# Kernel optimization log

Hardware: AMD Instinct MI355X
Metric: run time of the kernel (lower is better)

The kernel has to match this reference:

```python
import jax, jax.numpy as jnp
import numpy as np

STATE_DIM = 64   # state_dim (N), N/2 complex modes
KLEN = 128       # L, learned impulse-response length
CH = 1           # channel_dim
BATCH = 32
T = 1048576      # sequence length (T > L -> FFT branch)
DT_MIN, DT_MAX = 0.001, 0.1


def setup_inputs() -> dict:
    key = jax.random.key(0)
    ks = jax.random.split(key, 7)
    N2 = STATE_DIM // 2
    x = jax.random.normal(ks[0], (BATCH, CH, T), dtype=jnp.float32)
    # HiPPO initialization: w = -0.5 + i * (1/pi) * N * (N/(1+2k) - 1)
    k = np.arange(N2)
    w_real = np.broadcast_to(np.float32(-0.5), (CH, N2)).copy()
    w_imag = np.broadcast_to(
        ((1.0 / np.pi) * STATE_DIM * (STATE_DIM / (1.0 + 2.0 * k) - 1.0)).astype(np.float32),
        (CH, N2)).copy()
    log_dt = (jax.random.uniform(ks[1], (CH, 1), dtype=jnp.float32)
              * (np.log(DT_MAX) - np.log(DT_MIN)) + np.log(DT_MIN))
    C_real = jax.random.normal(ks[2], (CH, 1, N2), dtype=jnp.float32) * 0.1
    C_imag = jax.random.normal(ks[3], (CH, 1, N2), dtype=jnp.float32) * 0.1
    B_real = jax.random.normal(ks[4], (CH, N2), dtype=jnp.float32)
    B_imag = jax.random.normal(ks[5], (CH, N2), dtype=jnp.float32)
    nrm = jnp.sqrt(jnp.sum(B_real ** 2 + B_imag ** 2, axis=-1, keepdims=True))
    B_real, B_imag = B_real / nrm, B_imag / nrm
    D = jax.random.normal(ks[6], (CH,), dtype=jnp.float32) * 0.1
    return {"azimuth_data": x,
            "w_real": jnp.asarray(w_real), "w_imag": jnp.asarray(w_imag),
            "log_dt": log_dt,
            "C_real": C_real, "C_imag": C_imag,
            "B_real": B_real, "B_imag": B_imag,
            "D": D}


def _ssm_kernel(w_real, w_imag, log_dt, C_real, C_imag, B_real, B_imag, D, L):
    """Vectorized equivalent of the per-step power recurrence: h_k = Re(sum_n C_n B_n A_n^k)."""
    w = w_real + 1j * w_imag                      # (CH, N2) complex eigenvalues
    dt = jnp.exp(log_dt)                          # (CH, 1)
    Cc = C_real + 1j * C_imag                     # (CH, 1, N2)
    Bc = B_real + 1j * B_imag                     # (CH, N2)
    dtA = dt[..., None] * w                       # (CH,1,1)*(CH,N2) -> (CH,1,N2)
    # coefficients C.squeeze(1) * B, with the same broadcast as torch: (CH,N2)*(CH,1,N2)->(CH,1,N2)
    coef = jnp.squeeze(Cc, axis=1) * (jnp.ones_like(dtA) * Bc)   # (CH,1,N2)
    ks = jnp.arange(L, dtype=dtA.real.dtype)                      # (L,)
    Ak = jnp.exp(dtA[..., None] * ks)                             # (CH,1,N2,L) = A_discrete**k
    h = jnp.real(jnp.sum(coef[..., None] * Ak, axis=-2))          # (CH,1,L)
    h = h.at[..., 0].add(D)                                       # hk[0] += D (broadcast (CH,1)+(CH,))
    return h[:, None]                                             # unsqueeze(1) -> (CH,1,1,L)


def reference(azimuth_data, w_real, w_imag, log_dt, C_real, C_imag, B_real, B_imag, D):
    Bsz, Cn, Tn = azimuth_data.shape
    kernel = _ssm_kernel(w_real, w_imag, log_dt, C_real, C_imag, B_real, B_imag, D, KLEN)
    pad = KLEN - 1
    x_padded = jnp.pad(azimuth_data, ((0, 0), (0, 0), (pad, 0)))   # causal left-pad
    L_conv = x_padded.shape[-1]
    x_f = jnp.fft.rfft(x_padded, n=L_conv)                         # (B, CH, F)
    k_f = jnp.fft.rfft(kernel, n=L_conv)                           # (CH, 1, 1, F)
    y_f = x_f * k_f                                                # broadcast -> (CH, B, 1, F)
    focused = jnp.fft.irfft(y_f, n=L_conv)[..., :Tn]               # (CH, B, 1, T) — matches torch broadcast
    return focused
```

## Files before the change

kernel.cpp:

```cpp
#include <hip/hip_runtime.h>

#define T_LEN  1048576
#define NROWS  32
#define NTAPS  128
#define N2     32
#define BLOCK  256
#define SEG    4096
#define SEGS_PER_ROW 256
#define HALO   256
#define NCH    11
#define STG_CH 1088

typedef __attribute__((ext_vector_type(8)))  _Float16 half8;
typedef __attribute__((ext_vector_type(2)))  __fp16   fp16x2;
typedef __attribute__((ext_vector_type(16))) float    f32x16;

__device__ __forceinline__ int swz(int q) { return q ^ ((q >> 3) & 7); }

__device__ __forceinline__ void gload_lds16(const float* g, float* l) {
  __builtin_amdgcn_global_load_lds(
      (const __attribute__((address_space(1))) void*)g,
      (__attribute__((address_space(3))) void*)l, 16, 0, 0);
}

__global__ __launch_bounds__(NTAPS) void ssm_taps(
    const float* __restrict__ w_real, const float* __restrict__ w_imag,
    const float* __restrict__ log_dt,
    const float* __restrict__ C_real, const float* __restrict__ C_imag,
    const float* __restrict__ B_real, const float* __restrict__ B_imag,
    const float* __restrict__ Dp, float* __restrict__ ws) {
  __shared__ float hsh[NTAPS];
  const int k = threadIdx.x;
  const float dt = expf(log_dt[0]);
  const float kf = (float)k;
  float acc = 0.f;
  for (int n = 0; n < N2; ++n) {
    const float a  = dt * w_real[n];
    const float b  = dt * w_imag[n];
    const float cr = C_real[n], ci = C_imag[n];
    const float br = B_real[n], bi = B_imag[n];
    const float coef_r = cr * br - ci * bi;
    const float coef_i = cr * bi + ci * br;
    const float e = expf(a * kf);
    float s, c;
    sincosf(b * kf, &s, &c);
    acc += e * (coef_r * c - coef_i * s);
  }
  if (k == 0) acc += Dp[0];
  ws[k]  = acc;
  hsh[k] = acc;
  __syncthreads();
  if (k < 64) {
    _Float16* AH = (_Float16*)(ws + NTAPS);
    const int m = k & 31, g = k >> 5;
    for (int c = 0; c < NCH; ++c)
      for (int i = 0; i < 8; ++i) {
        const int idx = m + 129 - 16 * c - 8 * g - i;
        const float v = (idx >= 0 && idx < NTAPS) ? hsh[idx] : 0.f;
        AH[(c * 64 + k) * 8 + i] = (_Float16)v;
      }
  }
}

__global__ __launch_bounds__(BLOCK, 8) void ssm_conv(
    const float* __restrict__ x, const float* __restrict__ ws,
    float* __restrict__ out) {
  __shared__ __align__(16) float lds[STG_CH * 4];

  const int tid  = threadIdx.x;
  const int lane = tid & 63;
  const int wid  = tid >> 6;
  const int p    = lane & 31, g = lane >> 5;
  const int row  = blockIdx.x >> 8;
  const int jb   = blockIdx.x & 255;
  const int n0   = jb * SEG;
  const float* __restrict__ xrow = x + (size_t)row * T_LEN;
  const half8* __restrict__ wsA = (const half8*)(ws + NTAPS);

#pragma unroll
  for (int j = 0; j < 5; ++j) {
    const int ch = j * 256 + wid * 64 + lane;
    if (ch < STG_CH) {
      int gfi = n0 - HALO + 4 * swz(ch);
      gfi = gfi < 0 ? 0 : gfi;
      gload_lds16(xrow + gfi, &lds[(j * 256 + wid * 64) * 4]);
    }
  }
  asm volatile("s_waitcnt vmcnt(0)" ::: "memory");
  __syncthreads();

  f32x16 acc = {};
#pragma unroll
  for (int c = 0; c < NCH; ++c) {
    const half8 A = wsA[c * 64 + lane];
    const int q0 = wid * 256 + 8 * p + 2 * g + 4 * c;
    const float4 f0 = *(const float4*)(lds + (swz(q0) << 2));
    const float4 f1 = *(const float4*)(lds + (swz(q0 + 1) << 2));
    union { half8 h8; unsigned u[4]; } bu;
    bu.u[0] = __builtin_bit_cast(unsigned, __builtin_amdgcn_cvt_pkrtz(f0.x, f0.y));
    bu.u[1] = __builtin_bit_cast(unsigned, __builtin_amdgcn_cvt_pkrtz(f0.z, f0.w));
    bu.u[2] = __builtin_bit_cast(unsigned, __builtin_amdgcn_cvt_pkrtz(f1.x, f1.y));
    bu.u[3] = __builtin_bit_cast(unsigned, __builtin_amdgcn_cvt_pkrtz(f1.z, f1.w));
    acc = __builtin_amdgcn_mfma_f32_32x32x16_f16(A, bu.h8, acc, 0, 0, 0);
  }

  float* __restrict__ orow =
      out + (size_t)row * T_LEN + n0 + wid * 1024 + 32 * p + 4 * g;
#pragma unroll
  for (int kq = 0; kq < 4; ++kq) {
    float4 v;
    v.x = acc[4 * kq];     v.y = acc[4 * kq + 1];
    v.z = acc[4 * kq + 2]; v.w = acc[4 * kq + 3];
    *(float4*)(orow + 8 * kq) = v;
  }
}

__global__ __launch_bounds__(BLOCK) void ssm_fix(
    const float* __restrict__ x, const float* __restrict__ ws,
    float* __restrict__ out) {
  const int row = blockIdx.x;
  const int n = threadIdx.x;
  const float* __restrict__ h = ws;
  const float* __restrict__ xrow = x + (size_t)row * T_LEN;
  float acc = 0.f;
  if (n < 127) {
    for (int k = n + 1; k < NTAPS; ++k)
      acc += h[k] * xrow[T_LEN + n - k];
  } else if (n < 254) {
    for (int k = 0; k <= n - 127; ++k)
      acc += h[k] * xrow[n - 127 - k];
  } else {
    return;
  }
  out[(size_t)row * T_LEN + n] = acc;
}

extern "C" void kernel_launch(void* const* d_in, const int* in_sizes, int n_in,
                              void* d_out, int out_size, void* d_ws, size_t ws_size,
                              hipStream_t stream) {
  const float* x      = (const float*)d_in[0];
  const float* w_real = (const float*)d_in[1];
  const float* w_imag = (const float*)d_in[2];
  const float* log_dt = (const float*)d_in[3];
  const float* C_real = (const float*)d_in[4];
  const float* C_imag = (const float*)d_in[5];
  const float* B_real = (const float*)d_in[6];
  const float* B_imag = (const float*)d_in[7];
  const float* Dp     = (const float*)d_in[8];
  float* out = (float*)d_out;
  float* ws  = (float*)d_ws;

  ssm_taps<<<1, NTAPS, 0, stream>>>(w_real, w_imag, log_dt,
                                    C_real, C_imag, B_real, B_imag, Dp, ws);
  ssm_conv<<<NROWS * SEGS_PER_ROW, BLOCK, 0, stream>>>(x, ws, out);
  ssm_fix<<<NROWS, BLOCK, 0, stream>>>(x, ws, out);
}
```

Measured before the change: 74.36 us.

## Stage tap matrix in LDS and transpose output through LDS for coalesced stores

The conv kernel now copies the fp16 Toeplitz tap fragments into LDS with a single wavefront's global_load_lds, instead of each lane loading them from global memory on its own. After the MFMA loop the accumulator tile is written to a padded LDS buffer and read back transposed, so each lane stores contiguous float4s across the full 1024-element span of its wave. This should give fully coalesced output writes. The costs are an extra barrier, more LDS per block (28 KB), and launch bounds lowered from 8 to 4 waves per EU, which may reduce occupancy.

```diff
diff --git a/kernel.cpp b/kernel.cpp
--- a/kernel.cpp
+++ b/kernel.cpp
@@ -17,7 +17,7 @@
 
 __device__ __forceinline__ int swz(int q) { return q ^ ((q >> 3) & 7); }
 
-__device__ __forceinline__ void gload_lds16(const float* g, float* l) {
+__device__ __forceinline__ void gload_lds16(const void* g, void* l) {
   __builtin_amdgcn_global_load_lds(
       (const __attribute__((address_space(1))) void*)g,
       (__attribute__((address_space(3))) void*)l, 16, 0, 0);
@@ -62,10 +62,12 @@
   }
 }
 
-__global__ __launch_bounds__(BLOCK, 8) void ssm_conv(
+__global__ __launch_bounds__(BLOCK, 4) void ssm_conv(
     const float* __restrict__ x, const float* __restrict__ ws,
     float* __restrict__ out) {
-  __shared__ __align__(16) float lds[STG_CH * 4];
+  __shared__ __align__(16) unsigned char smem[28672];
+  float*    xs   = (float*)smem;
+  _Float16* ldsA = (_Float16*)(smem + 17408);
 
   const int tid  = threadIdx.x;
   const int lane = tid & 63;
@@ -75,7 +77,6 @@
   const int jb   = blockIdx.x & 255;
   const int n0   = jb * SEG;
   const float* __restrict__ xrow = x + (size_t)row * T_LEN;
-  const half8* __restrict__ wsA = (const half8*)(ws + NTAPS);
 
 #pragma unroll
   for (int j = 0; j < 5; ++j) {
@@ -83,8 +84,14 @@
     if (ch < STG_CH) {
       int gfi = n0 - HALO + 4 * swz(ch);
       gfi = gfi < 0 ? 0 : gfi;
-      gload_lds16(xrow + gfi, &lds[(j * 256 + wid * 64) * 4]);
+      gload_lds16(xrow + gfi, xs + (j * 256 + wid * 64) * 4);
     }
+  }
+  if (wid == 0) {
+    const _Float16* gA = (const _Float16*)(ws + NTAPS);
+#pragma unroll
+    for (int c = 0; c < NCH; ++c)
+      gload_lds16(gA + (c * 64 + lane) * 8, ldsA + c * 512);
   }
   asm volatile("s_waitcnt vmcnt(0)" ::: "memory");
   __syncthreads();
@@ -92,10 +99,10 @@
   f32x16 acc = {};
 #pragma unroll
   for (int c = 0; c < NCH; ++c) {
-    const half8 A = wsA[c * 64 + lane];
+    const half8 A = *(const half8*)(ldsA + c * 512 + lane * 8);
     const int q0 = wid * 256 + 8 * p + 2 * g + 4 * c;
-    const float4 f0 = *(const float4*)(lds + (swz(q0) << 2));
-    const float4 f1 = *(const float4*)(lds + (swz(q0 + 1) << 2));
+    const float4 f0 = *(const float4*)(xs + (swz(q0) << 2));
+    const float4 f1 = *(const float4*)(xs + (swz(q0 + 1) << 2));
     union { half8 h8; unsigned u[4]; } bu;
     bu.u[0] = __builtin_bit_cast(unsigned, __builtin_amdgcn_cvt_pkrtz(f0.x, f0.y));
     bu.u[1] = __builtin_bit_cast(unsigned, __builtin_amdgcn_cvt_pkrtz(f0.z, f0.w));
@@ -104,14 +111,25 @@
     acc = __builtin_amdgcn_mfma_f32_32x32x16_f16(A, bu.h8, acc, 0, 0, 0);
   }
 
-  float* __restrict__ orow =
-      out + (size_t)row * T_LEN + n0 + wid * 1024 + 32 * p + 4 * g;
+  __syncthreads();
+  float* ebuf = (float*)smem;
+  const int wr = wid * 1056;
 #pragma unroll
-  for (int kq = 0; kq < 4; ++kq) {
+  for (int r = 0; r < 16; ++r) {
+    const int m = (r & 3) + 8 * (r >> 2) + 4 * g;
+    ebuf[wr + m * 33 + p] = acc[r];
+  }
+  float* __restrict__ obase = out + (size_t)row * T_LEN + n0 + wid * 1024;
+#pragma unroll
+  for (int pp = 0; pp < 4; ++pp) {
+    const int o  = 4 * lane + 256 * pp;
+    const int m0 = o & 31, pc = o >> 5;
     float4 v;
-    v.x = acc[4 * kq];     v.y = acc[4 * kq + 1];
-    v.z = acc[4 * kq + 2]; v.w = acc[4 * kq + 3];
-    *(float4*)(orow + 8 * kq) = v;
+    v.x = ebuf[wr + (m0 + 0) * 33 + pc];
+    v.y = ebuf[wr + (m0 + 1) * 33 + pc];
+    v.z = ebuf[wr + (m0 + 2) * 33 + pc];
+    v.w = ebuf[wr + (m0 + 3) * 33 + pc];
+    *(float4*)(obase + o) = v;
   }
 }
 
```

Result: faster. 71.37 us (-4.0%).

## Stage input as fp16 in LDS, preload taps, transpose epilogue, fuse fixup

Applied to the files above, without the earlier changes.

The input tile is loaded into registers, converted to fp16 and stored in a swizzled LDS layout, replacing the direct global-to-LDS fp32 copy. The MFMA B operand is then read with a single 16-byte LDS load and no per-chunk conversion. The filter fragments are preloaded into registers before the loop. The accumulator is transposed through LDS so output stores are fully coalesced, and the wrap-around fixup kernel is folded into the jb==0 blocks, removing one launch. The cost is more registers, reflected in the occupancy hint dropping from 8 to 5, an extra barrier, and a serial tail in the first block of each row.

```diff
diff --git a/kernel.cpp b/kernel.cpp
--- a/kernel.cpp
+++ b/kernel.cpp
@@ -9,19 +9,15 @@
 #define SEGS_PER_ROW 256
 #define HALO   256
 #define NCH    11
-#define STG_CH 1088
+#define STG_F32 (SEG + HALO)
+#define STG_Q4  (STG_F32 / 4)
+#define EPI_F32 (32 * 36)
 
 typedef __attribute__((ext_vector_type(8)))  _Float16 half8;
 typedef __attribute__((ext_vector_type(2)))  __fp16   fp16x2;
 typedef __attribute__((ext_vector_type(16))) float    f32x16;
 
-__device__ __forceinline__ int swz(int q) { return q ^ ((q >> 3) & 7); }
-
-__device__ __forceinline__ void gload_lds16(const float* g, float* l) {
-  __builtin_amdgcn_global_load_lds(
-      (const __attribute__((address_space(1))) void*)g,
-      (__attribute__((address_space(3))) void*)l, 16, 0, 0);
-}
+__device__ __forceinline__ int swz16(int q) { return q ^ ((q >> 3) & 7); }
 
 __global__ __launch_bounds__(NTAPS) void ssm_taps(
     const float* __restrict__ w_real, const float* __restrict__ w_imag,
@@ -62,10 +58,10 @@
   }
 }
 
-__global__ __launch_bounds__(BLOCK, 8) void ssm_conv(
+__global__ __launch_bounds__(BLOCK, 5) void ssm_conv(
     const float* __restrict__ x, const float* __restrict__ ws,
     float* __restrict__ out) {
-  __shared__ __align__(16) float lds[STG_CH * 4];
+  __shared__ __align__(16) unsigned char smem[4 * EPI_F32 * 4];
 
   const int tid  = threadIdx.x;
   const int lane = tid & 63;
@@ -75,64 +71,72 @@
   const int jb   = blockIdx.x & 255;
   const int n0   = jb * SEG;
   const float* __restrict__ xrow = x + (size_t)row * T_LEN;
+
+  half8 A[NCH];
   const half8* __restrict__ wsA = (const half8*)(ws + NTAPS);
+#pragma unroll
+  for (int c = 0; c < NCH; ++c) A[c] = wsA[c * 64 + lane];
 
+  _Float16* xh = (_Float16*)smem;
 #pragma unroll
   for (int j = 0; j < 5; ++j) {
-    const int ch = j * 256 + wid * 64 + lane;
-    if (ch < STG_CH) {
-      int gfi = n0 - HALO + 4 * swz(ch);
+    const int q4 = tid + 256 * j;
+    if (q4 < STG_Q4) {
+      int gfi = n0 - HALO + 4 * q4;
       gfi = gfi < 0 ? 0 : gfi;
-      gload_lds16(xrow + gfi, &lds[(j * 256 + wid * 64) * 4]);
+      const float4 f = *(const float4*)(xrow + gfi);
+      const fp16x2 a = __builtin_amdgcn_cvt_pkrtz(f.x, f.y);
+      const fp16x2 b = __builtin_amdgcn_cvt_pkrtz(f.z, f.w);
+      uint2 w;
+      w.x = __builtin_bit_cast(unsigned, a);
+      w.y = __builtin_bit_cast(unsigned, b);
+      const int c16 = q4 >> 1;
+      *(uint2*)((char*)xh + swz16(c16) * 16 + (q4 & 1) * 8) = w;
     }
   }
-  asm volatile("s_waitcnt vmcnt(0)" ::: "memory");
   __syncthreads();
 
+  const int qb = wid * 128 + 4 * p + g;
   f32x16 acc = {};
 #pragma unroll
   for (int c = 0; c < NCH; ++c) {
-    const half8 A = wsA[c * 64 + lane];
-    const int q0 = wid * 256 + 8 * p + 2 * g + 4 * c;
-    const float4 f0 = *(const float4*)(lds + (swz(q0) << 2));
-    const float4 f1 = *(const float4*)(lds + (swz(q0 + 1) << 2));
-    union { half8 h8; unsigned u[4]; } bu;
-    bu.u[0] = __builtin_bit_cast(unsigned, __builtin_amdgcn_cvt_pkrtz(f0.x, f0.y));
-    bu.u[1] = __builtin_bit_cast(unsigned, __builtin_amdgcn_cvt_pkrtz(f0.z, f0.w));
-    bu.u[2] = __builtin_bit_cast(unsigned, __builtin_amdgcn_cvt_pkrtz(f1.x, f1.y));
-    bu.u[3] = __builtin_bit_cast(unsigned, __builtin_amdgcn_cvt_pkrtz(f1.z, f1.w));
-    acc = __builtin_amdgcn_mfma_f32_32x32x16_f16(A, bu.h8, acc, 0, 0, 0);
+    const half8 B = *(const half8*)((char*)xh + swz16(qb + 2 * c) * 16);
+    acc = __builtin_amdgcn_mfma_f32_32x32x16_f16(A[c], B, acc, 0, 0, 0);
+  }
+  __syncthreads();
+
+  float* ebuf = (float*)smem + wid * EPI_F32;
+#pragma unroll
+  for (int k = 0; k < 4; ++k) {
+    float4 v;
+    v.x = acc[4 * k];     v.y = acc[4 * k + 1];
+    v.z = acc[4 * k + 2]; v.w = acc[4 * k + 3];
+    *(float4*)(ebuf + p * 36 + 8 * k + 4 * g) = v;
+  }
+  float* __restrict__ obase = out + (size_t)row * T_LEN + n0 + wid * 1024;
+#pragma unroll
+  for (int pp = 0; pp < 4; ++pp) {
+    const int o  = 4 * lane + 256 * pp;
+    const int m0 = o & 31, pc = o >> 5;
+    const float4 v = *(const float4*)(ebuf + pc * 36 + m0);
+    *(float4*)(obase + o) = v;
   }
 
-  float* __restrict__ orow =
-      out + (size_t)row * T_LEN + n0 + wid * 1024 + 32 * p + 4 * g;
-#pragma unroll
-  for (int kq = 0; kq < 4; ++kq) {
-    float4 v;
-    v.x = acc[4 * kq];     v.y = acc[4 * kq + 1];
-    v.z = acc[4 * kq + 2]; v.w = acc[4 * kq + 3];
-    *(float4*)(orow + 8 * kq) = v;
+  if (jb == 0) {
+    __syncthreads();
+    const float* __restrict__ h = ws;
+    if (tid < 254) {
+      float a = 0.f;
+      if (tid < 127) {
+        for (int k = tid + 1; k < NTAPS; ++k)
+          a += h[k] * xrow[T_LEN + tid - k];
+      } else {
+        for (int k = 0; k <= tid - 127; ++k)
+          a += h[k] * xrow[tid - 127 - k];
+      }
+      out[(size_t)row * T_LEN + tid] = a;
+    }
   }
-}
-
-__global__ __launch_bounds__(BLOCK) void ssm_fix(
-    const float* __restrict__ x, const float* __restrict__ ws,
-    float* __restrict__ out) {
-  const int row = blockIdx.x;
-  const int n = threadIdx.x;
-  const float* __restrict__ h = ws;
-  const float* __restrict__ xrow = x + (size_t)row * T_LEN;
-  float acc = 0.f;
-  if (n < 127) {
-    for (int k = n + 1; k < NTAPS; ++k)
-      acc += h[k] * xrow[T_LEN + n - k];
-  } else if (n < 254) {
-    for (int k = 0; k <= n - 127; ++k)
-      acc += h[k] * xrow[n - 127 - k];
-  } else {
-    return;
-  }
-  out[(size_t)row * T_LEN + n] = acc;
 }
 
 extern "C" void kernel_launch(void* const* d_in, const int* in_sizes, int n_in,
@@ -153,5 +157,4 @@
   ssm_taps<<<1, NTAPS, 0, stream>>>(w_real, w_imag, log_dt,
                                     C_real, C_imag, B_real, B_imag, Dp, ws);
   ssm_conv<<<NROWS * SEGS_PER_ROW, BLOCK, 0, stream>>>(x, ws, out);
-  ssm_fix<<<NROWS, BLOCK, 0, stream>>>(x, ws, out);
 }
```

New measurement: 65.75 us. -11.6%, faster.
